# Optimization experiments

Measured on AMD Instinct MI355X. Metric: run time of the kernel, lower is better.

## Reference

```python
import jax, jax.numpy as jnp
import numpy as np

ANG = 7; C = 32; H = 32; W = 32; B = 4
E = 4 * C; HEADS = 4; NV = ANG * 32; TOK = C * NV; HID = int(C * 2.66)


def _ln(x, g, b, eps=1e-6):
    m = x.mean(-1, keepdims=True)
    v = ((x - m) ** 2).mean(-1, keepdims=True)
    return (x - m) * jax.lax.rsqrt(v + eps) * g + b


def _ln_nchw(x, g, b):
    return _ln(x.transpose(0, 2, 3, 1), g, b).transpose(0, 3, 1, 2)


def _l2(x):
    return x / jnp.maximum(jnp.linalg.norm(x, axis=-1, keepdims=True), 1e-12)


def _c11(w, x):  # 1x1 conv, w: [out, in]
    return jnp.einsum('oc,bchw->bohw', w, x)


def _dw3(x, w):  # depthwise 3x3, w: [Ch, 1, 3, 3]
    return jax.lax.conv_general_dilated(x, w, (1, 1), ((1, 1), (1, 1)),
                                        dimension_numbers=('NCHW', 'OIHW', 'NCHW'),
                                        feature_group_count=x.shape[1])


def _branch(buf, p):  # buf: [B, C, N, V, W]
    lin_w, temp, ln1_g, ln1_b, qkv_w, qkvdw_w, proj_w, attca_w, lne_g, lne_b, pin_w, dw_w, pout_w = p
    Bb, Cc, N, V, Wd = buf.shape
    L = V * Wd
    x_tok = buf.transpose(0, 3, 4, 1, 2).reshape(Bb, L, Cc * N) @ lin_w.T  # [B, L, E]
    x_res = buf.transpose(0, 2, 1, 3, 4).reshape(Bb * N, Cc, V, Wd)
    x = x_tok.reshape(Bb, V, Wd, E).transpose(0, 3, 1, 2)  # [B, E, V, W]
    qkv = _dw3(_c11(qkv_w, _ln_nchw(x, ln1_g, ln1_b)), qkvdw_w)
    q, k, v_ = jnp.split(qkv, 3, axis=1)
    d = E // HEADS
    to_heads = lambda t: t.reshape(Bb, HEADS, d, L).transpose(0, 1, 3, 2)  # [B, h, L, d]
    q, k, v_ = _l2(to_heads(q)), _l2(to_heads(k)), to_heads(v_)
    logits = jnp.einsum('bhld,bhmd->bhlm', q, k) * temp
    attn0 = jax.nn.softmax(logits, axis=-1)
    a1 = jnp.maximum(logits, 0.0) ** 2
    a1 = jax.nn.gelu(a1, approximate=False) * a1
    scale, shift = jnp.split(jnp.einsum('oh,bhlm->bolm', attca_w, a1), 2, axis=1)
    attn = attn0 * (1.0 + scale) + shift
    out = jnp.einsum('bhlm,bhmd->bhld', attn, v_).transpose(0, 1, 3, 2).reshape(Bb, E, V, Wd)
    out = _c11(proj_w, out).reshape(Bb, Cc, N, V, Wd).transpose(0, 2, 1, 3, 4).reshape(Bb * N, Cc, V, Wd)
    x = x_res + out
    h2 = _dw3(_c11(pin_w, _ln_nchw(x, lne_g, lne_b)), dw_w)
    h1, hg = jnp.split(h2, 2, axis=1)
    x = x + _c11(pout_w, jax.nn.gelu(h1, approximate=False) * hg)
    return x.reshape(Bb, N, Cc, V, Wd).transpose(0, 2, 1, 3, 4)


def _forward(x_lf, hp, vp, f1_w, f2_w):
    Bt = x_lf.shape[0]
    Bb = Bt // (ANG * ANG)
    x6 = x_lf.reshape(Bb, ANG, ANG, C, H, W)  # (b,u,v,c,h,w)
    epi1 = x6.transpose(0, 3, 2, 5, 1, 4).reshape(Bb, C, ANG * W, ANG, H)  # b c (v w) u h
    epi2 = x6.transpose(0, 3, 1, 4, 2, 5).reshape(Bb, C, ANG * H, ANG, W)  # b c (u h) v w
    o1 = _branch(epi1, hp).reshape(Bb, C, ANG, W, ANG, H).transpose(0, 4, 2, 1, 5, 3).reshape(Bt, C, H, W)
    o2 = _branch(epi2, vp).reshape(Bb, C, ANG, H, ANG, W).transpose(0, 2, 4, 1, 3, 5).reshape(Bt, C, H, W)
    g = jnp.concatenate([o1, o2], axis=1).max(axis=(2, 3))  # AdaptiveMaxPool2d(1) -> [Bt, 2C]
    g = g @ f1_w.T
    g = jnp.where(g >= 0, g, 0.1 * g)  # LeakyReLU(0.1)
    g = jax.nn.sigmoid(g @ f2_w.T)[:, :, None, None]
    return o1 * g + o2 * (1.0 - g)


def setup_inputs() -> dict:
    key = jax.random.key(0)
    ks = iter(jax.random.split(key, 64))
    rn = lambda shape: jax.random.normal(next(ks), shape, jnp.float32) * 0.02
    d = {"x_lf": jax.random.normal(next(ks), (B * ANG * ANG, C, H, W), jnp.float32)}
    for pref in ("h_", "v_"):
        d[pref + "lin_w"] = rn((E, TOK))
        d[pref + "temp"] = jnp.ones((1, HEADS, 1, 1), jnp.float32)
        d[pref + "ln1_g"] = jnp.ones((E,), jnp.float32)
        d[pref + "ln1_b"] = jnp.zeros((E,), jnp.float32)
        d[pref + "qkv_w"] = rn((3 * E, E))
        d[pref + "qkvdw_w"] = rn((3 * E, 1, 3, 3))
        d[pref + "proj_w"] = rn((TOK, E))
        d[pref + "attca_w"] = rn((2 * HEADS, HEADS))
        d[pref + "lne_g"] = jnp.ones((C,), jnp.float32)
        d[pref + "lne_b"] = jnp.zeros((C,), jnp.float32)
        d[pref + "pin_w"] = rn((2 * HID, C))
        d[pref + "dw_w"] = rn((2 * HID, 1, 3, 3))
        d[pref + "pout_w"] = rn((C, HID))
    d["f1_w"] = rn((C // 4, 2 * C))
    d["f2_w"] = rn((C, C // 4))
    return d


def reference(x_lf, h_lin_w, h_temp, h_ln1_g, h_ln1_b, h_qkv_w, h_qkvdw_w, h_proj_w, h_attca_w,
              h_lne_g, h_lne_b, h_pin_w, h_dw_w, h_pout_w,
              v_lin_w, v_temp, v_ln1_g, v_ln1_b, v_qkv_w, v_qkvdw_w, v_proj_w, v_attca_w,
              v_lne_g, v_lne_b, v_pin_w, v_dw_w, v_pout_w, f1_w, f2_w):
    hp = (h_lin_w, h_temp, h_ln1_g, h_ln1_b, h_qkv_w, h_qkvdw_w, h_proj_w, h_attca_w,
          h_lne_g, h_lne_b, h_pin_w, h_dw_w, h_pout_w)
    vp = (v_lin_w, v_temp, v_ln1_g, v_ln1_b, v_qkv_w, v_qkvdw_w, v_proj_w, v_attca_w,
          v_lne_g, v_lne_b, v_pin_w, v_dw_w, v_pout_w)
    return _forward(x_lf, hp, vp, f1_w, f2_w)
```

## Files before the change

### kernel.cpp

```cpp
#include <hip/hip_runtime.h>
#include <math.h>

typedef unsigned short u16;
typedef unsigned int   u32;
typedef __attribute__((ext_vector_type(8))) short short8;
typedef __attribute__((ext_vector_type(4))) short short4v;
typedef __attribute__((ext_vector_type(4))) float float4v;
typedef __attribute__((ext_vector_type(2))) float float2v;
typedef __attribute__((ext_vector_type(2))) unsigned int u32x2;

#define DI __device__ __forceinline__

DI float b2f(u16 v){ return __uint_as_float(((u32)v) << 16); }
DI u16 f2b(float f){
  u32 u = __float_as_uint(f);
  u32 r = (u + 0x7fffu + ((u >> 16) & 1u)) >> 16;
  return (u16)r;
}
DI float fast_gelu(float x){
  float ax = fabsf(x) * 0.70710678118654752f;
  float t  = __builtin_amdgcn_rcpf(fmaf(0.3275911f, ax, 1.0f));
  float p  = t * (0.254829592f + t * (-0.284496736f + t * (1.421413741f +
             t * (-1.453152027f + t * 1.061405429f))));
  float e  = __expf(-ax * ax);
  float ea = fmaf(-p, e, 1.0f);
  float er = (x >= 0.f) ? ea : -ea;
  return 0.5f * x * (1.0f + er);
}

DI float2v pk_fma(float2v a, float2v b, float2v c){
  float2v d;
  asm("v_pk_fma_f32 %0, %1, %2, %3" : "=v"(d) : "v"(a), "v"(b), "v"(c));
  return d;
}
DI u32 cvt_pk_bf16(float lo, float hi){
  u32 r;
  asm("v_cvt_pk_bf16_f32 %0, %1, %2" : "=v"(r) : "v"(lo), "v"(hi));
  return r;
}


__global__ __launch_bounds__(256) void k_prep(const float* __restrict__ lw0,
    const float* __restrict__ lw1, const float* __restrict__ pw0,
    const float* __restrict__ pw1,
    const float* __restrict__ pin0, const float* __restrict__ pin1,
    const float* __restrict__ po0,  const float* __restrict__ po1,
    const float* __restrict__ qw0,  const float* __restrict__ qw1,
    u16* __restrict__ linwB, u16* __restrict__ projB,
    u16* __restrict__ pinB, u16* __restrict__ poB, u16* __restrict__ qkvwB)
{
  if (blockIdx.x < 3584) {
    int base = blockIdx.x * 1024 + threadIdx.x;
    #pragma unroll
    for (int r = 0; r < 4; ++r) {
      int i = base + 256 * r;
      if (i < 1835008) {
        const float* src = (i < 917504) ? lw0 : lw1;
        linwB[i] = f2b(src[i % 917504]);
      } else if (i < 3670016) {
        int j = i - 1835008;
        const float* src = (j < 917504) ? pw0 : pw1;
        projB[j] = f2b(src[j % 917504]);
      }
    }
  } else {
    int idx = (blockIdx.x - 3584) * 256 + threadIdx.x;
    if (idx < 12288) {
      int cc = idx & 31;
      int r = (idx >> 5) % 96;
      int hb = (idx >> 5) / 96;
      int br = hb >> 1, half = hb & 1;
      const float* p = br ? pin1 : pin0;
      pinB[idx] = (r < 85) ? f2b(p[(half * 85 + r) * 32 + cc]) : (u16)0;
    } else if (idx < 18432) {
      int j = idx - 12288;
      int r = j % 96;
      int t = j / 96;
      int br = t >> 5, cc = t & 31;
      const float* p = br ? po1 : po0;
      poB[j] = (r < 85) ? f2b(p[cc * 85 + r]) : (u16)0;
    } else if (idx < 116736) {
      int j = idx - 18432;
      int br = j / 49152, rest = j % 49152;
      qkvwB[j] = f2b((br ? qw1 : qw0)[rest]);
    }
  }
}

__global__ __launch_bounds__(256) void k1_mfma(const float* __restrict__ xlf,
    const u16* __restrict__ linwB, float* __restrict__ xqp)
{
  __shared__ __align__(16) u16 Asb[64][40];
  __shared__ __align__(16) u16 Wsb[128][40];
  const int ks   = blockIdx.x;
  const int mblk = blockIdx.y;
  const int bb   = blockIdx.z;
  const int br = bb >> 2, b = bb & 3;
  const int tid = threadIdx.x;
  const int wid = tid >> 6, lane = tid & 63;
  const int quad = lane >> 4, r16 = lane & 15;
  const int m0s = mblk * 64 + wid * 16;
  const bool active = (m0s < 224);
  const u16* wsrc = linwB + br * 917504;
  const int c = ks;

  float4v acc[8];
  #pragma unroll
  for (int nt = 0; nt < 8; ++nt) acc[nt] = (float4v){0.f, 0.f, 0.f, 0.f};

  #pragma unroll 1
  for (int step = 0; step < 7; ++step) {
    const int k0 = ks * 224 + step * 32;
    #pragma unroll
    for (int r = 0; r < 2; ++r) {
      int idx = tid + 256 * r;
      if (br == 0) {
        int ml = idx >> 3, kl4 = idx & 7;
        int l = mblk * 64 + ml;
        float4v v4 = {0.f, 0.f, 0.f, 0.f};
        if (l < 224) {
          int u = l >> 5, h = l & 31;
          v4 = *(const float4v*)&xlf[(b * 49 + u * 7 + step) * 32768 + c * 1024 + h * 32 + kl4 * 4];
        }
        u32 lo = cvt_pk_bf16(v4[0], v4[1]);
        u32 hi = cvt_pk_bf16(v4[2], v4[3]);
        *(u32x2*)&Asb[ml][kl4 * 4] = (u32x2){lo, hi};
      } else {
        int ml4 = idx & 15, kl = idx >> 4;
        int ml0 = ml4 * 4;
        int l0 = mblk * 64 + ml0;
        float4v v4 = {0.f, 0.f, 0.f, 0.f};
        if (l0 < 224) {
          int v2 = l0 >> 5, w2 = l0 & 31;
          v4 = *(const float4v*)&xlf[(b * 49 + step * 7 + v2) * 32768 + c * 1024 + kl * 32 + w2];
        }
        Asb[ml0 + 0][kl] = f2b(v4[0]);
        Asb[ml0 + 1][kl] = f2b(v4[1]);
        Asb[ml0 + 2][kl] = f2b(v4[2]);
        Asb[ml0 + 3][kl] = f2b(v4[3]);
      }
    }
    #pragma unroll
    for (int r = 0; r < 4; ++r) {
      int idx = tid + 256 * r;
      int e = idx >> 3, kl4 = idx & 7;
      *(short4v*)&Wsb[e][kl4 * 4] = *(const short4v*)&wsrc[e * 7168 + k0 + kl4 * 4];
    }
    __syncthreads();
    if (active) {
      short8 af = *(const short8*)&Asb[wid * 16 + r16][quad * 8];
      #pragma unroll
      for (int nt = 0; nt < 8; ++nt) {
        short8 bf = *(const short8*)&Wsb[nt * 16 + r16][quad * 8];
        acc[nt] = __builtin_amdgcn_mfma_f32_16x16x32_bf16(af, bf, acc[nt], 0, 0, 0);
      }
    }
    __syncthreads();
  }
  if (active) {
    float* outp = xqp + ks * 229376 + (bb * 224 + m0s) * 128;
    #pragma unroll
    for (int nt = 0; nt < 8; ++nt) {
      int e = nt * 16 + r16;
      #pragma unroll
      for (int reg = 0; reg < 4; ++reg) {
        int tok = quad * 4 + reg;
        outp[tok * 128 + e] = acc[nt][reg];
      }
    }
  }
}

__global__ __launch_bounds__(256) void k1b_ln(const float* __restrict__ xqp,
    const float* __restrict__ g0, const float* __restrict__ b0,
    const float* __restrict__ g1, const float* __restrict__ b1,
    u16* __restrict__ xn)
{
  const int tid = threadIdx.x;
  const int row = blockIdx.x * 16 + (tid >> 4);
  const int p = tid & 15;
  const int bb = row / 224;
  const int br = bb >> 2;
  const float* lg = br ? g1 : g0;
  const float* lb = br ? b1 : b0;
  const int e0 = p * 8;
  float4v a0 = {0.f,0.f,0.f,0.f}, a1 = {0.f,0.f,0.f,0.f};
  const float* src = xqp + row * 128 + e0;
  #pragma unroll
  for (int ks = 0; ks < 32; ++ks) {
    const float4v* sp = (const float4v*)(src + ks * 229376);
    a0 += sp[0];
    a1 += sp[1];
  }
  float s = 0.f, s2 = 0.f;
  #pragma unroll
  for (int j = 0; j < 4; ++j) {
    s  += a0[j] + a1[j];
    s2 += a0[j] * a0[j] + a1[j] * a1[j];
  }
  #pragma unroll
  for (int m = 8; m >= 1; m >>= 1) {
    s  += __shfl_xor(s, m);
    s2 += __shfl_xor(s2, m);
  }
  float mean = s * (1.f / 128.f);
  float var  = s2 * (1.f / 128.f) - mean * mean;
  float rs   = rsqrtf(fmaxf(var, 0.f) + 1e-6f);
  u16 o[8];
  #pragma unroll
  for (int j = 0; j < 4; ++j) {
    o[j]     = f2b((a0[j] - mean) * rs * lg[e0 + j]     + lb[e0 + j]);
    o[4 + j] = f2b((a1[j] - mean) * rs * lg[e0 + 4 + j] + lb[e0 + 4 + j]);
  }
  *(short8*)&xn[row * 128 + e0] = *(const short8*)o;
}

__global__ __launch_bounds__(256) void k3_mfma(const u16* __restrict__ xn,
    const u16* __restrict__ qkvwB, float* __restrict__ qkvp)
{
  const int mchunk = blockIdx.x;
  const int nh = blockIdx.y;
  const int bb = blockIdx.z;
  const int br = bb >> 2;
  const int tid = threadIdx.x;
  const int wid = tid >> 6, lane = tid & 63;
  const int quad = lane >> 4, r16 = lane & 15;

  const int mtile = mchunk * 64 + wid * 16;
  const u16* wsrc = qkvwB + br * 49152;
  const u16* bsrc = xn + (bb * 224 + nh * 112) * 128;
  float4v acc[7];
  #pragma unroll
  for (int nt = 0; nt < 7; ++nt) acc[nt] = (float4v){0.f, 0.f, 0.f, 0.f};
  #pragma unroll
  for (int k = 0; k < 4; ++k) {
    short8 af = *(const short8*)&wsrc[(mtile + r16) * 128 + k * 32 + quad * 8];
    #pragma unroll
    for (int nt = 0; nt < 7; ++nt) {
      short8 bf = *(const short8*)&bsrc[(nt * 16 + r16) * 128 + k * 32 + quad * 8];
      acc[nt] = __builtin_amdgcn_mfma_f32_16x16x32_bf16(af, bf, acc[nt], 0, 0, 0);
    }
  }
  #pragma unroll
  for (int nt = 0; nt < 7; ++nt) {
    int tok = nh * 112 + nt * 16 + r16;
    #pragma unroll
    for (int reg = 0; reg < 4; ++reg) {
      int o = mtile + quad * 4 + reg;
      qkvp[(bb * 384 + o) * 224 + tok] = acc[nt][reg];
    }
  }
}

__global__ __launch_bounds__(256) void k45_dwheads(const float* __restrict__ qkvp,
    const float* __restrict__ dw0, const float* __restrict__ dw1,
    float* __restrict__ qkvn)
{
  __shared__ float ps[32][161];
  __shared__ float ts[32][137];
  __shared__ float scs[128];
  const int bid = blockIdx.x;
  const int half = bid & 1;
  const int rest = bid >> 1;
  const int h = rest & 3;
  const int sel = (rest >> 2) % 3;
  const int bb = rest / 12;
  const int br = bb >> 2;
  const int tid = threadIdx.x;
  const int o0 = sel * 128 + h * 32;
  const float* src = qkvp + (bb * 384 + o0) * 224;
  const float* dwa = (br ? dw1 : dw0) + o0 * 9;
  const int vin0  = half ? 3 : 0;
  const int nin   = half ? 128 : 160;
  const int vout0 = half ? 4 : 0;
  const int nout  = half ? 96 : 128;
  const int lout0 = vout0 * 32;
  for (int idx = tid; idx < 32 * nin; idx += 256) {
    int d = idx / nin, l = idx - d * nin;
    ps[d][l] = src[d * 224 + vin0 * 32 + l];
  }
  __syncthreads();
  for (int idx = tid; idx < 32 * nout; idx += 256) {
    int d = idx / nout, lo = idx - d * nout;
    int l = lout0 + lo;
    int v = l >> 5, w = l & 31;
    const float* dww = dwa + d * 9;
    float acc = 0.f;
    #pragma unroll
    for (int dy = -1; dy <= 1; ++dy) {
      int vv = v + dy; if (vv < 0 || vv > 6) continue;
      int vloc = vv - vin0;
      #pragma unroll
      for (int dx = -1; dx <= 1; ++dx) {
        int ww = w + dx; if (ww < 0 || ww > 31) continue;
        acc += ps[d][vloc * 32 + ww] * dww[(dy + 1) * 3 + (dx + 1)];
      }
    }
    ts[d][lo] = acc;
  }
  __syncthreads();
  if (tid < nout) {
    float ss = 0.f;
    #pragma unroll 8
    for (int d = 0; d < 32; ++d) { float x = ts[d][tid]; ss += x * x; }
    scs[tid] = (sel < 2) ? (1.0f / fmaxf(sqrtf(ss), 1e-12f)) : 1.0f;
  }
  __syncthreads();
  float* dst = qkvn + ((bb * 3 + sel) * 4 + h) * 7168;
  for (int idx = tid; idx < 32 * nout; idx += 256) {
    int d = idx & 31, lo = idx >> 5;
    dst[(lout0 + lo) * 32 + d] = ts[d][lo] * scs[lo];
  }
}

__global__ __launch_bounds__(256) void k6_attn(const float* __restrict__ qkvn,
    const float* __restrict__ tmp0, const float* __restrict__ tmp1,
    const float* __restrict__ ca0,  const float* __restrict__ ca1,
    u16* __restrict__ aoB)
{
  __shared__ float qs[16][33];
  __shared__ float ks[128][33];
  __shared__ float sS[16 * 228];
  __shared__ float mxs[16], rss[16];
  __shared__ float caf[32], tpf[4];
  const int it = blockIdx.x;
  const int b = blockIdx.y, br = blockIdx.z;
  const int bb = br * 4 + b;
  const int tid = threadIdx.x;
  const float* tw = br ? tmp1 : tmp0;
  const float* cw = br ? ca1 : ca0;
  if (tid < 32) caf[tid] = cw[tid];
  if (tid < 4)  tpf[tid] = tw[tid];
  const int i0 = it * 4;
  const float* qb = qkvn + (bb * 3 + 0) * 4 * 7168;
  const float* kb = qkvn + (bb * 3 + 1) * 4 * 7168;
  const float* vb = qkvn + (bb * 3 + 2) * 4 * 7168;
  #pragma unroll
  for (int r = 0; r < 2; ++r) {
    int idx = tid + 256 * r;
    if (idx < 512) {
      int d = idx & 31, i = (idx >> 5) & 3, h = idx >> 7;
      qs[h * 4 + i][d] = qb[h * 7168 + (i0 + i) * 32 + d];
    }
  }
  __syncthreads();
  const int hC = tid >> 6, iC = (tid >> 4) & 3, jq = tid & 15;
  float qv[32];
  #pragma unroll
  for (int d2 = 0; d2 < 32; ++d2) qv[d2] = qs[hC * 4 + iC][d2];
  for (int jt = 0; jt < 7; ++jt) {
    __syncthreads();
    #pragma unroll
    for (int r = 0; r < 16; ++r) {
      int idx = tid + 256 * r;
      int d = idx & 31, jj = (idx >> 5) & 31, h = idx >> 10;
      ks[h * 32 + jj][d] = kb[h * 7168 + (jt * 32 + jj) * 32 + d];
    }
    __syncthreads();
    float a2[2] = {0.f, 0.f};
    for (int d = 0; d < 32; ++d) {
      #pragma unroll
      for (int r = 0; r < 2; ++r) a2[r] += qv[d] * ks[hC * 32 + jq + 16 * r][d];
    }
    #pragma unroll
    for (int r = 0; r < 2; ++r)
      sS[(hC * 4 + iC) * 228 + jt * 32 + jq + 16 * r] = a2[r] * tpf[hC];
  }
  __syncthreads();
  {
    int p = tid & 15, row = tid >> 4;
    float mx = -1e30f;
    for (int q = 0; q < 14; ++q) mx = fmaxf(mx, sS[row * 228 + p + 16 * q]);
    #pragma unroll
    for (int m = 8; m >= 1; m >>= 1) mx = fmaxf(mx, __shfl_xor(mx, m));
    float es = 0.f;
    for (int q = 0; q < 14; ++q) es += __expf(sS[row * 228 + p + 16 * q] - mx);
    #pragma unroll
    for (int m = 8; m >= 1; m >>= 1) es += __shfl_xor(es, m);
    if (p == 0) { mxs[row] = mx; rss[row] = 1.0f / es; }
  }
  __syncthreads();
  for (int q = 0; q < 4; ++q) {
    int pr = tid + 256 * q;
    if (pr < 896) {
      int i = pr / 224, j = pr % 224;
      float a1[4];
      #pragma unroll
      for (int hh = 0; hh < 4; ++hh) {
        float sv = sS[(hh * 4 + i) * 228 + j];
        float z = fmaxf(sv, 0.f); float z2 = z * z;
        a1[hh] = fast_gelu(z2) * z2;
      }
      #pragma unroll
      for (int hh = 0; hh < 4; ++hh) {
        float sc = 0.f, sh = 0.f;
        #pragma unroll
        for (int k2 = 0; k2 < 4; ++k2) { sc += caf[hh * 4 + k2] * a1[k2]; sh += caf[(hh + 4) * 4 + k2] * a1[k2]; }
        int row = hh * 4 + i;
        float at = __expf(sS[row * 228 + j] - mxs[row]) * rss[row];
        sS[row * 228 + j] = at * (1.f + sc) + sh;
      }
    }
  }
  __syncthreads();
  {
    int d = tid & 31, hpair = (tid >> 5) & 1, rg = tid >> 6;
    float acc[2] = {0.f, 0.f};
    for (int jt = 0; jt < 7; ++jt) {
      __syncthreads();
      #pragma unroll
      for (int r = 0; r < 16; ++r) {
        int idx = tid + 256 * r;
        int dd = idx & 31, jj = (idx >> 5) & 31, hh2 = idx >> 10;
        ks[hh2 * 32 + jj][dd] = vb[hh2 * 7168 + (jt * 32 + jj) * 32 + dd];
      }
      __syncthreads();
      for (int j = 0; j < 32; ++j) {
        #pragma unroll
        for (int c2 = 0; c2 < 2; ++c2) {
          int hh = hpair * 2 + c2;
          acc[c2] += sS[(hh * 4 + rg) * 228 + jt * 32 + j] * ks[hh * 32 + j][d];
        }
      }
    }
    #pragma unroll
    for (int c2 = 0; c2 < 2; ++c2) {
      int hh = hpair * 2 + c2;
      aoB[(bb * 224 + i0 + rg) * 128 + hh * 32 + d] = f2b(acc[c2]);
    }
  }
}

__global__ __launch_bounds__(256) void k7_mfma(const u16* __restrict__ aoB,
    const u16* __restrict__ projB, const float* __restrict__ xlf, u16* __restrict__ x2)
{
  __shared__ float Ts[64][68];
  const int mchunk = blockIdx.x;
  const int mi = blockIdx.y;
  const int bb = blockIdx.z;
  const int br = bb >> 2, b = bb & 3;
  const int tid = threadIdx.x;
  const int wid = tid >> 6, lane = tid & 63;
  const int quad = lane >> 4, r16 = lane & 15;
  const u16* asrc = projB + br * 917504;
  const u16* bsrc = aoB + bb * 224 * 128;
  const int mbase = mchunk * 256 + (wid * 4 + mi) * 16;
  float4v acc[14];
  #pragma unroll
  for (int nt = 0; nt < 14; ++nt) acc[nt] = (float4v){0.f, 0.f, 0.f, 0.f};
  #pragma unroll
  for (int k = 0; k < 4; ++k) {
    short8 af = *(const short8*)&asrc[(mbase + r16) * 128 + k * 32 + quad * 8];
    #pragma unroll
    for (int nt = 0; nt < 14; ++nt) {
      short8 bf = *(const short8*)&bsrc[(nt * 16 + r16) * 128 + k * 32 + quad * 8];
      acc[nt] = __builtin_amdgcn_mfma_f32_16x16x32_bf16(af, bf, acc[nt], 0, 0, 0);
    }
  }
  #pragma unroll
  for (int rd = 0; rd < 4; ++rd) {
    const int ntn = (rd < 3) ? 4 : 2;
    __syncthreads();
    #pragma unroll
    for (int t = 0; t < 4; ++t) {
      if (t < ntn) {
        #pragma unroll
        for (int reg = 0; reg < 4; ++reg)
          Ts[wid * 16 + quad * 4 + reg][t * 16 + r16] = acc[rd * 4 + t][reg];
      }
    }
    __syncthreads();
    const int nq = ntn * 4;
    #pragma unroll
    for (int pass = 0; pass < 4; ++pass) {
      int idx = tid + 256 * pass;
      if (idx < 64 * nq) {
        int rloc = idx / nq;
        int qc = idx - rloc * nq;
        int row = mchunk * 256 + (((rloc >> 4) * 4 + mi) << 4) + (rloc & 15);
        int c = row / 224, n = row - c * 224;
        int l = rd * 64 + qc * 4;
        float4v tv = *(const float4v*)&Ts[rloc][qc * 4];
        float r0v, r1v, r2v, r3v;
        if (br == 0) {
          int img = b * 49 + (l >> 5) * 7 + (n >> 5);
          const float* xp = xlf + img * 32768 + c * 1024 + (l & 31) * 32 + (n & 31);
          r0v = xp[0]; r1v = xp[32]; r2v = xp[64]; r3v = xp[96];
        } else {
          int img = b * 49 + (n >> 5) * 7 + (l >> 5);
          float4v xv = *(const float4v*)(xlf + img * 32768 + c * 1024 + (n & 31) * 32 + (l & 31));
          r0v = xv[0]; r1v = xv[1]; r2v = xv[2]; r3v = xv[3];
        }
        u32 lo = cvt_pk_bf16(tv[0] + r0v, tv[1] + r1v);
        u32 hi = cvt_pk_bf16(tv[2] + r2v, tv[3] + r3v);
        u16* dp = &x2[(((br * 896 + b * 224 + n) * 32 + c) << 8) + l];
        *(u32x2*)dp = (u32x2){lo, hi};
      }
    }
  }
}

__global__ __launch_bounds__(256, 4) void k8_mfma(u16* x2,
    const float* __restrict__ lg0, const float* __restrict__ lb0,
    const float* __restrict__ lg1, const float* __restrict__ lb1,
    const float* __restrict__ dwa0, const float* __restrict__ dwa1,
    const u16* __restrict__ pinB, const u16* __restrict__ poB)
{
  __shared__ __align__(16) u16 xnb[224][36];
  __shared__ __align__(16) u32 t12[16][231];
  __shared__ __align__(16) u16 gsb[224][20];
  const int img = blockIdx.x;
  const int br  = blockIdx.y;
  const float* lg  = br ? lg1 : lg0;
  const float* lb  = br ? lb1 : lb0;
  const float* dww = br ? dwa1 : dwa0;
  const u16* pinBr = pinB + br * 2 * 96 * 32;
  const u16* poBr  = poB + br * 32 * 96;
  const int tid = threadIdx.x;
  const int wid = tid >> 6, lane = tid & 63;
  const int quad = lane >> 4, r16 = lane & 15;
  u16* src = x2 + (br * 896 + img) * 8192;

  if (tid < 224) {
    float xr[32];
    #pragma unroll
    for (int cc = 0; cc < 32; ++cc) xr[cc] = b2f(src[cc * 256 + tid]);
    float s = 0.f, s2 = 0.f;
    #pragma unroll
    for (int cc = 0; cc < 32; ++cc) { s += xr[cc]; s2 += xr[cc] * xr[cc]; }
    float mean = s * (1.f / 32.f);
    float var  = s2 * (1.f / 32.f) - mean * mean;
    float rs   = rsqrtf(fmaxf(var, 0.f) + 1e-6f);
    #pragma unroll
    for (int cc = 0; cc < 32; ++cc)
      xnb[tid][cc] = f2b((xr[cc] - mean) * rs * lg[cc] + lb[cc]);
  }
  __syncthreads();

  float4v acc[7];
  #pragma unroll
  for (int i = 0; i < 7; ++i) acc[i] = (float4v){0.f, 0.f, 0.f, 0.f};

  #pragma unroll 1
  for (int it = 0; it < 6; ++it) {
    const int r0 = it * 16;
    #pragma unroll
    for (int ni = 0; ni < 4; ++ni) {
      int n = wid + 4 * ni;
      if (n < 14) {
        const int tok = n * 16 + r16;
        short8 bf;
        const u16* xp = &xnb[tok][quad * 8];
        ((short4v*)&bf)[0] = *(const short4v*)xp;
        ((short4v*)&bf)[1] = *(const short4v*)(xp + 4);
        short8 af0 = *(const short8*)&pinBr[((r0 + r16) << 5) + quad * 8];
        short8 af1 = *(const short8*)&pinBr[((96 + r0 + r16) << 5) + quad * 8];
        float4v d0 = __builtin_amdgcn_mfma_f32_16x16x32_bf16(af0, bf,
                       (float4v){0.f, 0.f, 0.f, 0.f}, 0, 0, 0);
        float4v d1 = __builtin_amdgcn_mfma_f32_16x16x32_bf16(af1, bf,
                       (float4v){0.f, 0.f, 0.f, 0.f}, 0, 0, 0);
        const int col = tok + (tok >> 5);
        #pragma unroll
        for (int reg = 0; reg < 4; ++reg)
          t12[quad * 4 + reg][col] = cvt_pk_bf16(d0[reg], d1[reg]);
      }
    }
    if (it > 0) {
      const int koff = (it - 1) * 16;
      #pragma unroll
      for (int i = 0; i < 7; ++i) {
        int u = wid + 4 * i;
        int mt = u / 14, n = u - mt * 14;
        short8 af = {}, bf = {};
        if (quad < 2) {
          af = *(const short8*)&poBr[(mt * 16 + r16) * 96 + koff + quad * 8];
          const u16* gp = &gsb[n * 16 + r16][quad * 8];
          ((short4v*)&bf)[0] = *(const short4v*)gp;
          ((short4v*)&bf)[1] = *(const short4v*)(gp + 4);
        }
        acc[i] = __builtin_amdgcn_mfma_f32_16x16x32_bf16(af, bf, acc[i], 0, 0, 0);
      }
    }
    __syncthreads();
    if (tid < 224) {
      const int rl = tid & 15;
      const int v  = tid >> 5;
      const int wh = (tid >> 4) & 1;
      const int r  = r0 + rl;
      float2v wp[9];
      if (r < 85) {
        const float* w1 = dww + r * 9;
        const float* w2 = dww + (85 + r) * 9;
        #pragma unroll
        for (int t = 0; t < 9; ++t) wp[t] = (float2v){w1[t], w2[t]};
      } else {
        #pragma unroll
        for (int t = 0; t < 9; ++t) wp[t] = (float2v){0.f, 0.f};
      }
      const u32* trow = &t12[rl][0];
      const int c0 = v * 33;
      const int base = wh << 4;
      const bool vok0 = (v > 0), vok2 = (v < 6);
      float2v accP = {0.f, 0.f}, accC = {0.f, 0.f}, accN = {0.f, 0.f};
      #pragma unroll
      for (int it2 = 0; it2 < 18; ++it2) {
        bool cok = true;
        if (it2 == 0)  cok = (wh == 1);
        if (it2 == 17) cok = (wh == 0);
        if (cok) {
          const int cw = base - 1 + it2;
          u32 p0 = vok0 ? trow[c0 - 33 + cw] : 0u;
          u32 p1 =        trow[c0 + cw];
          u32 p2 = vok2 ? trow[c0 + 33 + cw] : 0u;
          float2v x0 = {__uint_as_float(p0 << 16), __uint_as_float(p0 & 0xffff0000u)};
          float2v x1 = {__uint_as_float(p1 << 16), __uint_as_float(p1 & 0xffff0000u)};
          float2v x2v = {__uint_as_float(p2 << 16), __uint_as_float(p2 & 0xffff0000u)};
          accP = pk_fma(x0, wp[2], accP);
          accC = pk_fma(x0, wp[1], accC);
          accN = pk_fma(x0, wp[0], accN);
          accP = pk_fma(x1, wp[5], accP);
          accC = pk_fma(x1, wp[4], accC);
          accN = pk_fma(x1, wp[3], accN);
          accP = pk_fma(x2v, wp[8], accP);
          accC = pk_fma(x2v, wp[7], accC);
          accN = pk_fma(x2v, wp[6], accN);
        }
        if (it2 >= 2) {
          float g = fast_gelu(accP[0]) * accP[1];
          gsb[(v << 5) + base + (it2 - 2)][rl] = f2b(g);
        }
        accP = accC; accC = accN; accN = (float2v){0.f, 0.f};
      }
    }
    __syncthreads();
  }
  {
    const int koff = 80;
    #pragma unroll
    for (int i = 0; i < 7; ++i) {
      int u = wid + 4 * i;
      int mt = u / 14, n = u - mt * 14;
      short8 af = {}, bf = {};
      if (quad < 2) {
        af = *(const short8*)&poBr[(mt * 16 + r16) * 96 + koff + quad * 8];
        const u16* gp = &gsb[n * 16 + r16][quad * 8];
        ((short4v*)&bf)[0] = *(const short4v*)gp;
        ((short4v*)&bf)[1] = *(const short4v*)(gp + 4);
      }
      acc[i] = __builtin_amdgcn_mfma_f32_16x16x32_bf16(af, bf, acc[i], 0, 0, 0);
    }
  }
  #pragma unroll
  for (int i = 0; i < 7; ++i) {
    int u = wid + 4 * i;
    int mt = u / 14, n = u - mt * 14;
    #pragma unroll
    for (int reg = 0; reg < 4; ++reg) {
      int cc = mt * 16 + quad * 4 + reg;
      int tok = n * 16 + r16;
      int o = cc * 256 + tok;
      src[o] = f2b(b2f(src[o]) + acc[i][reg]);
    }
  }
}

__global__ __launch_bounds__(256) void k9_pool(const u16* __restrict__ x3, float* __restrict__ gmax)
{
  __shared__ float red[4];
  const int bid = blockIdx.x;
  const int c64 = bid & 63;
  const int t = bid >> 6;
  const int c = c64 & 31, which = c64 >> 5;
  const int b = t / 49; const int uv = t % 49; const int u = uv / 7; const int vq = uv % 7;
  const int tid = threadIdx.x;
  float mx = -1e30f;
  if (which == 0) {
    int h = tid & 31, w0 = tid >> 5;
    #pragma unroll
    for (int r = 0; r < 4; ++r) {
      int w = w0 + 8 * r;
      mx = fmaxf(mx, b2f(x3[((b * 224 + vq * 32 + w) * 32 + c) * 256 + u * 32 + h]));
    }
  } else {
    int w = tid & 31, h0 = tid >> 5;
    #pragma unroll
    for (int r = 0; r < 4; ++r) {
      int h = h0 + 8 * r;
      mx = fmaxf(mx, b2f(x3[((896 + b * 224 + u * 32 + h) * 32 + c) * 256 + vq * 32 + w]));
    }
  }
  #pragma unroll
  for (int m = 32; m >= 1; m >>= 1) mx = fmaxf(mx, __shfl_xor(mx, m));
  if ((tid & 63) == 0) red[tid >> 6] = mx;
  __syncthreads();
  if (tid == 0)
    gmax[t * 64 + c64] = fmaxf(fmaxf(red[0], red[1]), fmaxf(red[2], red[3]));
}

__global__ __launch_bounds__(256) void k9_final(const u16* __restrict__ x3,
    const float* __restrict__ gmax, const float* __restrict__ f1,
    const float* __restrict__ f2, float* __restrict__ out)
{
  __shared__ float o1s[32][33];
  __shared__ float g1s[8];
  __shared__ float gs;
  const int bid = blockIdx.x;
  const int c = bid & 31;
  const int t = bid >> 5;
  const int b = t / 49; const int uv = t % 49; const int u = uv / 7; const int vq = uv % 7;
  const int tid = threadIdx.x;
  #pragma unroll
  for (int r = 0; r < 4; ++r) {
    int h = tid & 31; int w = (tid >> 5) + 8 * r;
    o1s[w][h] = b2f(x3[((b * 224 + vq * 32 + w) * 32 + c) * 256 + u * 32 + h]);
  }
  if (tid < 8) {
    float a = 0.f;
    for (int c2 = 0; c2 < 64; ++c2) a += f1[tid * 64 + c2] * gmax[t * 64 + c2];
    g1s[tid] = (a >= 0.f) ? a : 0.1f * a;
  }
  __syncthreads();
  if (tid == 0) {
    float a = 0.f;
    #pragma unroll
    for (int o = 0; o < 8; ++o) a += f2[c * 8 + o] * g1s[o];
    gs = 1.f / (1.f + expf(-a));
  }
  __syncthreads();
  const float g = gs;
  #pragma unroll
  for (int r = 0; r < 4; ++r) {
    int w = tid & 31; int h = (tid >> 5) + 8 * r;
    float o2 = b2f(x3[((896 + b * 224 + u * 32 + h) * 32 + c) * 256 + vq * 32 + w]);
    float o1 = o1s[w][h];
    out[(t * 32 + c) * 1024 + h * 32 + w] = o1 * g + o2 * (1.f - g);
  }
}

extern "C" void kernel_launch(void* const* d_in, const int* in_sizes, int n_in,
                              void* d_out, int out_size, void* d_ws, size_t ws_size,
                              hipStream_t stream)
{
  const float* xlf    = (const float*)d_in[0];
  const float* h_lin  = (const float*)d_in[1];
  const float* h_temp = (const float*)d_in[2];
  const float* h_g1   = (const float*)d_in[3];
  const float* h_b1   = (const float*)d_in[4];
  const float* h_qkv  = (const float*)d_in[5];
  const float* h_qdw  = (const float*)d_in[6];
  const float* h_proj = (const float*)d_in[7];
  const float* h_ca   = (const float*)d_in[8];
  const float* h_ge   = (const float*)d_in[9];
  const float* h_be   = (const float*)d_in[10];
  const float* h_pin  = (const float*)d_in[11];
  const float* h_dw   = (const float*)d_in[12];
  const float* h_po   = (const float*)d_in[13];
  const float* v_lin  = (const float*)d_in[14];
  const float* v_temp = (const float*)d_in[15];
  const float* v_g1   = (const float*)d_in[16];
  const float* v_b1   = (const float*)d_in[17];
  const float* v_qkv  = (const float*)d_in[18];
  const float* v_qdw  = (const float*)d_in[19];
  const float* v_proj = (const float*)d_in[20];
  const float* v_ca   = (const float*)d_in[21];
  const float* v_ge   = (const float*)d_in[22];
  const float* v_be   = (const float*)d_in[23];
  const float* v_pin  = (const float*)d_in[24];
  const float* v_dw   = (const float*)d_in[25];
  const float* v_po   = (const float*)d_in[26];
  const float* f1     = (const float*)d_in[27];
  const float* f2     = (const float*)d_in[28];

  char* w = (char*)d_ws;
  u16*   x2    = (u16*)  (w + 0);
  float* xqp   = (float*)(w + 0);
  float* qkvp  = (float*)(w + 29360128);
  float* qkvn  = (float*)(w + 32112640);
  float* gmax  = (float*)(w + 34865152);
  u16*   pinB  = (u16*)  (w + 34940416);
  u16*   poB   = (u16*)  (w + 34964992);
  u16*   qkvwB = (u16*)  (w + 34977280);
  u16*   aoB   = (u16*)  (w + 35173888);
  u16*   linwB = (u16*)  (w + 35632640);
  u16*   projB = (u16*)  (w + 39302656);
  u16*   xn    = (u16*)  (w + 42972672);

  k_prep   <<<4040, 256, 0, stream>>>(h_lin, v_lin, h_proj, v_proj,
                                      h_pin, v_pin, h_po, v_po, h_qkv, v_qkv,
                                      linwB, projB, pinB, poB, qkvwB);
  k1_mfma  <<<dim3(32, 4, 8), 256, 0, stream>>>(xlf, linwB, xqp);
  k1b_ln   <<<112, 256, 0, stream>>>(xqp, h_g1, h_b1, v_g1, v_b1, xn);
  k3_mfma  <<<dim3(6, 2, 8), 256, 0, stream>>>(xn, qkvwB, qkvp);
  k45_dwheads <<<192, 256, 0, stream>>>(qkvp, h_qdw, v_qdw, qkvn);
  k6_attn  <<<dim3(56, 4, 2), 256, 0, stream>>>(qkvn, h_temp, v_temp, h_ca, v_ca, aoB);
  k7_mfma  <<<dim3(28, 4, 8), 256, 0, stream>>>(aoB, projB, xlf, x2);
  k8_mfma  <<<dim3(896, 2), 256, 0, stream>>>(x2, h_ge, h_be, v_ge, v_be,
                                              h_dw, v_dw, pinB, poB);
  k9_pool  <<<12544, 256, 0, stream>>>(x2, gmax);
  k9_final <<<6272, 256, 0, stream>>>(x2, gmax, f1, f2, (float*)d_out);
}
```

Baseline: 412.7 us.

## Fuse max-pool into k8 epilogue via atomics; stage B operands in LDS

Removes the separate k9_pool kernel by computing per-channel maxima inside k8's epilogue. It uses an order-preserving uint encoding with shared-memory atomicMax, then global atomicMax into a gmax buffer that k_prep zero-initialises. It also stages the B operand (xn / aoB) into LDS in k3 and k7 instead of re-reading it from global memory per MFMA. The cost is atomic contention, extra LDS use (which may reduce occupancy in k7), and an added barrier in k8.

```diff
diff --git a/kernel.cpp b/kernel.cpp
--- a/kernel.cpp
+++ b/kernel.cpp
@@ -17,6 +17,8 @@
   u32 r = (u + 0x7fffu + ((u >> 16) & 1u)) >> 16;
   return (u16)r;
 }
+DI u32 ford(u32 u){ return ((int)u < 0) ? ~u : (u | 0x80000000u); }
+DI float fdec(u32 m){ u32 u = (m & 0x80000000u) ? (m ^ 0x80000000u) : ~m; return __uint_as_float(u); }
 DI float fast_gelu(float x){
   float ax = fabsf(x) * 0.70710678118654752f;
   float t  = __builtin_amdgcn_rcpf(fmaf(0.3275911f, ax, 1.0f));
@@ -47,7 +49,8 @@
     const float* __restrict__ po0,  const float* __restrict__ po1,
     const float* __restrict__ qw0,  const float* __restrict__ qw1,
     u16* __restrict__ linwB, u16* __restrict__ projB,
-    u16* __restrict__ pinB, u16* __restrict__ poB, u16* __restrict__ qkvwB)
+    u16* __restrict__ pinB, u16* __restrict__ poB, u16* __restrict__ qkvwB,
+    u32* __restrict__ gmaxU)
 {
   if (blockIdx.x < 3584) {
     int base = blockIdx.x * 1024 + threadIdx.x;
@@ -63,7 +66,7 @@
         projB[j] = f2b(src[j % 917504]);
       }
     }
-  } else {
+  } else if (blockIdx.x < 4040) {
     int idx = (blockIdx.x - 3584) * 256 + threadIdx.x;
     if (idx < 12288) {
       int cc = idx & 31;
@@ -84,6 +87,9 @@
       int br = j / 49152, rest = j % 49152;
       qkvwB[j] = f2b((br ? qw1 : qw0)[rest]);
     }
+  } else {
+    int idx = (blockIdx.x - 4040) * 256 + threadIdx.x;
+    if (idx < 12544) gmaxU[idx] = 0u;
   }
 }
 
@@ -218,6 +224,7 @@
 __global__ __launch_bounds__(256) void k3_mfma(const u16* __restrict__ xn,
     const u16* __restrict__ qkvwB, float* __restrict__ qkvp)
 {
+  __shared__ u16 xnb[112][140];
   const int mchunk = blockIdx.x;
   const int nh = blockIdx.y;
   const int bb = blockIdx.z;
@@ -226,9 +233,16 @@
   const int wid = tid >> 6, lane = tid & 63;
   const int quad = lane >> 4, r16 = lane & 15;
 
+  #pragma unroll
+  for (int i = 0; i < 7; ++i) {
+    int idx = tid + 256 * i;
+    int row = idx >> 4, c8 = idx & 15;
+    *(short8*)&xnb[row][c8 * 8] = *(const short8*)&xn[(bb * 224 + nh * 112 + row) * 128 + c8 * 8];
+  }
+  __syncthreads();
+
   const int mtile = mchunk * 64 + wid * 16;
   const u16* wsrc = qkvwB + br * 49152;
-  const u16* bsrc = xn + (bb * 224 + nh * 112) * 128;
   float4v acc[7];
   #pragma unroll
   for (int nt = 0; nt < 7; ++nt) acc[nt] = (float4v){0.f, 0.f, 0.f, 0.f};
@@ -237,7 +251,7 @@
     short8 af = *(const short8*)&wsrc[(mtile + r16) * 128 + k * 32 + quad * 8];
     #pragma unroll
     for (int nt = 0; nt < 7; ++nt) {
-      short8 bf = *(const short8*)&bsrc[(nt * 16 + r16) * 128 + k * 32 + quad * 8];
+      short8 bf = *(const short8*)&xnb[nt * 16 + r16][k * 32 + quad * 8];
       acc[nt] = __builtin_amdgcn_mfma_f32_16x16x32_bf16(af, bf, acc[nt], 0, 0, 0);
     }
   }
@@ -434,6 +448,7 @@
 __global__ __launch_bounds__(256) void k7_mfma(const u16* __restrict__ aoB,
     const u16* __restrict__ projB, const float* __restrict__ xlf, u16* __restrict__ x2)
 {
+  __shared__ u16 Bs[224][140];
   __shared__ float Ts[64][68];
   const int mchunk = blockIdx.x;
   const int mi = blockIdx.y;
@@ -443,7 +458,13 @@
   const int wid = tid >> 6, lane = tid & 63;
   const int quad = lane >> 4, r16 = lane & 15;
   const u16* asrc = projB + br * 917504;
-  const u16* bsrc = aoB + bb * 224 * 128;
+  #pragma unroll
+  for (int i = 0; i < 14; ++i) {
+    int idx = tid + 256 * i;
+    int row = idx >> 4, c8 = idx & 15;
+    *(short8*)&Bs[row][c8 * 8] = *(const short8*)&aoB[(bb * 224 + row) * 128 + c8 * 8];
+  }
+  __syncthreads();
   const int mbase = mchunk * 256 + (wid * 4 + mi) * 16;
   float4v acc[14];
   #pragma unroll
@@ -453,7 +474,7 @@
     short8 af = *(const short8*)&asrc[(mbase + r16) * 128 + k * 32 + quad * 8];
     #pragma unroll
     for (int nt = 0; nt < 14; ++nt) {
-      short8 bf = *(const short8*)&bsrc[(nt * 16 + r16) * 128 + k * 32 + quad * 8];
+      short8 bf = *(const short8*)&Bs[nt * 16 + r16][k * 32 + quad * 8];
       acc[nt] = __builtin_amdgcn_mfma_f32_16x16x32_bf16(af, bf, acc[nt], 0, 0, 0);
     }
   }
@@ -504,7 +525,8 @@
     const float* __restrict__ lg0, const float* __restrict__ lb0,
     const float* __restrict__ lg1, const float* __restrict__ lb1,
     const float* __restrict__ dwa0, const float* __restrict__ dwa1,
-    const u16* __restrict__ pinB, const u16* __restrict__ poB)
+    const u16* __restrict__ pinB, const u16* __restrict__ poB,
+    u32* __restrict__ gmaxU)
 {
   __shared__ __align__(16) u16 xnb[224][36];
   __shared__ __align__(16) u32 t12[16][231];
@@ -650,6 +672,9 @@
       acc[i] = __builtin_amdgcn_mfma_f32_16x16x32_bf16(af, bf, acc[i], 0, 0, 0);
     }
   }
+  u32* pm = (u32*)t12;
+  for (int idx2 = tid; idx2 < 224; idx2 += 256) pm[idx2] = 0u;
+  __syncthreads();
   #pragma unroll
   for (int i = 0; i < 7; ++i) {
     int u = wid + 4 * i;
@@ -659,46 +684,23 @@
       int cc = mt * 16 + quad * 4 + reg;
       int tok = n * 16 + r16;
       int o = cc * 256 + tok;
-      src[o] = f2b(b2f(src[o]) + acc[i][reg]);
-    }
-  }
-}
-
-__global__ __launch_bounds__(256) void k9_pool(const u16* __restrict__ x3, float* __restrict__ gmax)
-{
-  __shared__ float red[4];
-  const int bid = blockIdx.x;
-  const int c64 = bid & 63;
-  const int t = bid >> 6;
-  const int c = c64 & 31, which = c64 >> 5;
-  const int b = t / 49; const int uv = t % 49; const int u = uv / 7; const int vq = uv % 7;
-  const int tid = threadIdx.x;
-  float mx = -1e30f;
-  if (which == 0) {
-    int h = tid & 31, w0 = tid >> 5;
-    #pragma unroll
-    for (int r = 0; r < 4; ++r) {
-      int w = w0 + 8 * r;
-      mx = fmaxf(mx, b2f(x3[((b * 224 + vq * 32 + w) * 32 + c) * 256 + u * 32 + h]));
-    }
-  } else {
-    int w = tid & 31, h0 = tid >> 5;
-    #pragma unroll
-    for (int r = 0; r < 4; ++r) {
-      int h = h0 + 8 * r;
-      mx = fmaxf(mx, b2f(x3[((896 + b * 224 + u * 32 + h) * 32 + c) * 256 + vq * 32 + w]));
-    }
-  }
-  #pragma unroll
-  for (int m = 32; m >= 1; m >>= 1) mx = fmaxf(mx, __shfl_xor(mx, m));
-  if ((tid & 63) == 0) red[tid >> 6] = mx;
-  __syncthreads();
-  if (tid == 0)
-    gmax[t * 64 + c64] = fmaxf(fmaxf(red[0], red[1]), fmaxf(red[2], red[3]));
+      u16 h16 = f2b(b2f(src[o]) + acc[i][reg]);
+      src[o] = h16;
+      atomicMax(&pm[cc * 7 + (tok >> 5)], ford(((u32)h16) << 16));
+    }
+  }
+  __syncthreads();
+  if (tid < 224) {
+    int c = tid / 7, g = tid - c * 7;
+    int bq = img / 224, rem = img - bq * 224;
+    int t = br ? (bq * 49 + (rem >> 5) * 7 + g) : (bq * 49 + g * 7 + (rem >> 5));
+    int gidx = t * 64 + (br ? 32 + c : c);
+    atomicMax(&gmaxU[gidx], pm[tid]);
+  }
 }
 
 __global__ __launch_bounds__(256) void k9_final(const u16* __restrict__ x3,
-    const float* __restrict__ gmax, const float* __restrict__ f1,
+    const u32* __restrict__ gmaxU, const float* __restrict__ f1,
     const float* __restrict__ f2, float* __restrict__ out)
 {
   __shared__ float o1s[32][33];
@@ -716,7 +718,7 @@
   }
   if (tid < 8) {
     float a = 0.f;
-    for (int c2 = 0; c2 < 64; ++c2) a += f1[tid * 64 + c2] * gmax[t * 64 + c2];
+    for (int c2 = 0; c2 < 64; ++c2) a += f1[tid * 64 + c2] * fdec(gmaxU[t * 64 + c2]);
     g1s[tid] = (a >= 0.f) ? a : 0.1f * a;
   }
   __syncthreads();
@@ -776,7 +778,7 @@
   float* xqp   = (float*)(w + 0);
   float* qkvp  = (float*)(w + 29360128);
   float* qkvn  = (float*)(w + 32112640);
-  float* gmax  = (float*)(w + 34865152);
+  u32*   gmaxU = (u32*)  (w + 34865152);
   u16*   pinB  = (u16*)  (w + 34940416);
   u16*   poB   = (u16*)  (w + 34964992);
   u16*   qkvwB = (u16*)  (w + 34977280);
@@ -785,9 +787,9 @@
   u16*   projB = (u16*)  (w + 39302656);
   u16*   xn    = (u16*)  (w + 42972672);
 
-  k_prep   <<<4040, 256, 0, stream>>>(h_lin, v_lin, h_proj, v_proj,
+  k_prep   <<<4089, 256, 0, stream>>>(h_lin, v_lin, h_proj, v_proj,
                                       h_pin, v_pin, h_po, v_po, h_qkv, v_qkv,
-                                      linwB, projB, pinB, poB, qkvwB);
+                                      linwB, projB, pinB, poB, qkvwB, gmaxU);
   k1_mfma  <<<dim3(32, 4, 8), 256, 0, stream>>>(xlf, linwB, xqp);
   k1b_ln   <<<112, 256, 0, stream>>>(xqp, h_g1, h_b1, v_g1, v_b1, xn);
   k3_mfma  <<<dim3(6, 2, 8), 256, 0, stream>>>(xn, qkvwB, qkvp);
@@ -795,7 +797,6 @@
   k6_attn  <<<dim3(56, 4, 2), 256, 0, stream>>>(qkvn, h_temp, v_temp, h_ca, v_ca, aoB);
   k7_mfma  <<<dim3(28, 4, 8), 256, 0, stream>>>(aoB, projB, xlf, x2);
   k8_mfma  <<<dim3(896, 2), 256, 0, stream>>>(x2, h_ge, h_be, v_ge, v_be,
-                                              h_dw, v_dw, pinB, poB);
-  k9_pool  <<<12544, 256, 0, stream>>>(x2, gmax);
-  k9_final <<<6272, 256, 0, stream>>>(x2, gmax, f1, f2, (float*)d_out);
-}
+                                              h_dw, v_dw, pinB, poB, gmaxU);
+  k9_final <<<6272, 256, 0, stream>>>(x2, gmaxU, f1, f2, (float*)d_out);
+}
```

Result: faster. 383.3 us (-7.1%).
